# Performance work log

Measured on AMD Instinct MI355X. Metric: run time of the kernel, lower is better.

Reference implementation:

```python
import jax, jax.numpy as jnp
import numpy as np

KERNEL = 500
PAD_IDX = 256


def setup_inputs() -> dict:
    key = jax.random.key(0)
    ks = jax.random.split(key, 8)
    B, L = 8, 1_000_000
    x = jax.random.randint(ks[0], (B, L), 0, 257, dtype=jnp.int64)
    emb = jax.random.normal(ks[1], (257, 8), dtype=jnp.float32)
    emb = emb.at[PAD_IDX].set(0.0)  # padding_idx row is zero
    W1 = jax.random.normal(ks[2], (128, 8, KERNEL), dtype=jnp.float32) * 0.02
    b1 = jax.random.normal(ks[3], (128,), dtype=jnp.float32) * 0.02
    W2 = jax.random.normal(ks[4], (128, 8, KERNEL), dtype=jnp.float32) * 0.02
    b2 = jax.random.normal(ks[5], (128,), dtype=jnp.float32) * 0.02
    fcW = jax.random.normal(ks[6], (2, 128), dtype=jnp.float32) * 0.1
    fcb = jax.random.normal(ks[7], (2,), dtype=jnp.float32) * 0.1
    return {"x": x, "emb": emb, "W1": W1, "b1": b1, "W2": W2, "b2": b2, "fcW": fcW, "fcb": fcb}


def reference(x, emb, W1, b1, W2, b2, fcW, fcb):
    B, L = x.shape
    P = L // KERNEL  # non-overlapping patches (stride == kernel_size)
    # embedding with padding_idx semantics: output zero at pad positions
    e = emb[x] * (x != PAD_IDX)[..., None].astype(emb.dtype)  # [B, L, 8]
    patches = e.reshape(B, P, KERNEL, 8)                      # [B, P, K, C]
    # conv1d(k=stride=500) == patchified GEMM; weight layout [out, in, k]
    g1 = jnp.einsum('bpkc,ock->bpo', patches, W1) + b1        # [B, P, 128]
    g2 = jnp.einsum('bpkc,ock->bpo', patches, W2) + b2
    h = jax.nn.relu(g1 * jax.nn.sigmoid(g2))                  # GLU gate + relu
    m = jnp.max(h, axis=1)                                    # global max pool -> [B, 128]
    return m @ fcW.T + fcb                                    # [B, num_classes]
```

## Files before the change

### kernel.cpp

```cpp
#include <hip/hip_runtime.h>


typedef __attribute__((ext_vector_type(8))) short short8;
typedef __attribute__((ext_vector_type(4))) float f32x4;

__device__ __forceinline__ unsigned short f2b(float f) {
    union { float f; unsigned u; } un;
    un.f = f;
    unsigned u = un.u;
    return (unsigned short)((u + 0x7FFFu + ((u >> 16) & 1u)) >> 16);
}

#define KT_COUNT 125
#define WS_BBLK_BYTES (KT_COUNT * 256 * 32 * 2)
#define WS_MWS_OFF WS_BBLK_BYTES

__global__ __launch_bounds__(128) void prep_weights(
        const float* __restrict__ W1, const float* __restrict__ W2,
        unsigned short* __restrict__ Bblk, float* __restrict__ m_ws) {
    const int o  = blockIdx.x;
    const int kt = threadIdx.x;
    if (kt < KT_COUNT) {
        const float* W = (o < 128) ? W1 : W2;
        const int oo = o & 127;
        unsigned short v[32];
#pragma unroll
        for (int c = 0; c < 8; ++c) {
            float4 f = *(const float4*)&W[oo * 4000 + c * 500 + kt * 4];
            v[c]      = f2b(f.x);
            v[8 + c]  = f2b(f.y);
            v[16 + c] = f2b(f.z);
            v[24 + c] = f2b(f.w);
        }
        unsigned short* dst = Bblk + kt * 8192 + o * 32;
#pragma unroll
        for (int q = 0; q < 4; ++q) {
            uint4 p;
            p.x = (unsigned)v[q * 8 + 0] | ((unsigned)v[q * 8 + 1] << 16);
            p.y = (unsigned)v[q * 8 + 2] | ((unsigned)v[q * 8 + 3] << 16);
            p.z = (unsigned)v[q * 8 + 4] | ((unsigned)v[q * 8 + 5] << 16);
            p.w = (unsigned)v[q * 8 + 6] | ((unsigned)v[q * 8 + 7] << 16);
            *(uint4*)(dst + q * 8) = p;
        }
    }
    if (blockIdx.x == 0)
        for (int i = threadIdx.x; i < 8 * 128; i += 128) m_ws[i] = 0.f;
}

__global__ __launch_bounds__(512, 2) void malconv_main(
        const int* __restrict__ x, const float* __restrict__ emb,
        const float* __restrict__ b1, const float* __restrict__ b2,
        const unsigned short* __restrict__ Bblk, float* __restrict__ m_ws) {
    __shared__ __align__(16) unsigned short embb[257 * 8];
    __shared__ __align__(16) unsigned short Alds[2][64 * 40];
    __shared__ __align__(16) unsigned short xlds[64 * 500];

    const int t = threadIdx.x;
    const int m0 = blockIdx.x * 64;

    for (int e = t; e < 257 * 8; e += 512) embb[e] = f2b(emb[e]);
    {
        const int4* xg = (const int4*)(x + m0 * 500);
        for (int i = t; i < 8000; i += 512) {
            int4 v = xg[i];
            ushort4 s;
            s.x = (unsigned short)v.x; s.y = (unsigned short)v.y;
            s.z = (unsigned short)v.z; s.w = (unsigned short)v.w;
            *(ushort4*)&xlds[i * 4] = s;
        }
    }

    const int lane = t & 63, wave = t >> 6;
    const int quad = lane >> 4, l16 = lane & 15;
    const int mq   = wave >> 2, nq = wave & 3;

    const int ar = t >> 2, aj = t & 3;

    const unsigned short* bbase = Bblk + (nq * 32 + l16) * 32 + quad * 8;

    f32x4 acc[2][4];
#pragma unroll
    for (int mi = 0; mi < 2; ++mi)
#pragma unroll
        for (int ni = 0; ni < 4; ++ni) {
            f32x4 z = {0.f, 0.f, 0.f, 0.f};
            acc[mi][ni] = z;
        }

    __syncthreads();

    unsigned short xvn = 0;
    if (t < 256) {
        unsigned short xv = xlds[ar * 500 + aj];
        *(uint4*)&Alds[0][ar * 40 + aj * 8] = *(const uint4*)&embb[xv * 8];
        xvn = xlds[ar * 500 + 4 + aj];
    }
    short8 bcur[4], bnxt[4];
    bcur[0] = *(const short8*)(bbase);
    bcur[1] = *(const short8*)(bbase + 512);
    bcur[2] = *(const short8*)(bbase + 4096);
    bcur[3] = *(const short8*)(bbase + 4608);
    __syncthreads();

    for (int kt = 0; kt < KT_COUNT; ++kt) {
        const int cur = kt & 1;
        if (kt < KT_COUNT - 1) {
            const unsigned short* bb = bbase + (kt + 1) * 8192;
            bnxt[0] = *(const short8*)(bb);
            bnxt[1] = *(const short8*)(bb + 512);
            bnxt[2] = *(const short8*)(bb + 4096);
            bnxt[3] = *(const short8*)(bb + 4608);
        }
        short8 afrag[2];
#pragma unroll
        for (int mi = 0; mi < 2; ++mi)
            afrag[mi] = *(const short8*)
                &Alds[cur][(mq * 32 + mi * 16 + l16) * 40 + quad * 8];
        if (t < 256 && kt < KT_COUNT - 1) {
            *(uint4*)&Alds[cur ^ 1][ar * 40 + aj * 8] =
                *(const uint4*)&embb[xvn * 8];
            if (kt < KT_COUNT - 2) xvn = xlds[ar * 500 + (kt + 2) * 4 + aj];
        }
#pragma unroll
        for (int mi = 0; mi < 2; ++mi)
#pragma unroll
            for (int ni = 0; ni < 4; ++ni)
                acc[mi][ni] = __builtin_amdgcn_mfma_f32_16x16x32_bf16(
                    afrag[mi], bcur[ni], acc[mi][ni], 0, 0, 0);
#pragma unroll
        for (int ni = 0; ni < 4; ++ni) bcur[ni] = bnxt[ni];
        __syncthreads();
    }

    const int b0 = m0 / 2000;
    const int bsplit = (b0 + 1) * 2000;
    const bool crosses = (m0 + 63) >= bsplit;
#pragma unroll
    for (int ni = 0; ni < 2; ++ni) {
        int o = nq * 32 + ni * 16 + l16;
        float bb1 = b1[o], bb2 = b2[o];
        float mx0 = 0.f, mx1 = 0.f;
#pragma unroll
        for (int mi = 0; mi < 2; ++mi)
#pragma unroll
            for (int r = 0; r < 4; ++r) {
                int ml = mq * 32 + mi * 16 + quad * 4 + r;
                float g1 = acc[mi][ni][r] + bb1;
                float g2 = acc[mi][ni + 2][r] + bb2;
                float h = fmaxf(g1 / (1.f + __expf(-g2)), 0.f);
                if (m0 + ml >= bsplit) mx1 = fmaxf(mx1, h);
                else                   mx0 = fmaxf(mx0, h);
            }
        mx0 = fmaxf(mx0, __shfl_xor(mx0, 16));
        mx0 = fmaxf(mx0, __shfl_xor(mx0, 32));
        mx1 = fmaxf(mx1, __shfl_xor(mx1, 16));
        mx1 = fmaxf(mx1, __shfl_xor(mx1, 32));
        if (quad == 0) {
            atomicMax((int*)&m_ws[b0 * 128 + o], __float_as_int(mx0));
            if (crosses)
                atomicMax((int*)&m_ws[(b0 + 1) * 128 + o], __float_as_int(mx1));
        }
    }
}

__global__ void fc_kernel(const float* __restrict__ m_ws,
                          const float* __restrict__ fcW,
                          const float* __restrict__ fcb,
                          float* __restrict__ out) {
    int t = threadIdx.x;
    if (t < 16) {
        int b = t >> 1, j = t & 1;
        float s = 0.f;
        for (int o = 0; o < 128; ++o) s += m_ws[b * 128 + o] * fcW[j * 128 + o];
        out[t] = s + fcb[j];
    }
}

extern "C" void kernel_launch(void* const* d_in, const int* in_sizes, int n_in,
                              void* d_out, int out_size, void* d_ws, size_t ws_size,
                              hipStream_t stream) {
    const int*   x   = (const int*)d_in[0];
    const float* emb = (const float*)d_in[1];
    const float* W1  = (const float*)d_in[2];
    const float* b1  = (const float*)d_in[3];
    const float* W2  = (const float*)d_in[4];
    const float* b2  = (const float*)d_in[5];
    const float* fcW = (const float*)d_in[6];
    const float* fcb = (const float*)d_in[7];
    float* out = (float*)d_out;

    unsigned short* Bblk = (unsigned short*)d_ws;
    float* m_ws = (float*)((char*)d_ws + WS_MWS_OFF);

    prep_weights<<<256, 128, 0, stream>>>(W1, W2, Bblk, m_ws);
    malconv_main<<<250, 512, 0, stream>>>(x, emb, b1, b2, Bblk, m_ws);
    fc_kernel<<<1, 64, 0, stream>>>(m_ws, fcW, fcb, out);
}
```

Baseline: 151.4 us.

## Gather A fragments directly from LDS embedding table, drop per-iteration barrier

Each lane now looks up its MFMA A fragment straight from the bf16 embedding table in LDS, indexed by its own token, instead of staging the fragments through a shared double buffer. This removes the LDS write/read round trip and the __syncthreads in every K-step. The weight prefetch is deepened to two steps ahead, which costs more registers per thread. Each A fragment is now loaded by all 4 N-waves rather than once, so LDS gather traffic goes up.

```diff
diff --git a/kernel.cpp b/kernel.cpp
--- a/kernel.cpp
+++ b/kernel.cpp
@@ -52,7 +52,6 @@
         const float* __restrict__ b1, const float* __restrict__ b2,
         const unsigned short* __restrict__ Bblk, float* __restrict__ m_ws) {
     __shared__ __align__(16) unsigned short embb[257 * 8];
-    __shared__ __align__(16) unsigned short Alds[2][64 * 40];
     __shared__ __align__(16) unsigned short xlds[64 * 500];
 
     const int t = threadIdx.x;
@@ -74,7 +73,8 @@
     const int quad = lane >> 4, l16 = lane & 15;
     const int mq   = wave >> 2, nq = wave & 3;
 
-    const int ar = t >> 2, aj = t & 3;
+    const int xb0 = (mq * 32 + l16) * 500 + quad;
+    const int xb1 = xb0 + 16 * 500;
 
     const unsigned short* bbase = Bblk + (nq * 32 + l16) * 32 + quad * 8;
 
@@ -89,47 +89,46 @@
 
     __syncthreads();
 
-    unsigned short xvn = 0;
-    if (t < 256) {
-        unsigned short xv = xlds[ar * 500 + aj];
-        *(uint4*)&Alds[0][ar * 40 + aj * 8] = *(const uint4*)&embb[xv * 8];
-        xvn = xlds[ar * 500 + 4 + aj];
+    unsigned short xv0 = xlds[xb0], xv1 = xlds[xb1];
+    short8 acur0 = *(const short8*)&embb[xv0 * 8];
+    short8 acur1 = *(const short8*)&embb[xv1 * 8];
+    unsigned short xg0 = xlds[xb0 + 4],  xg1 = xlds[xb1 + 4];
+    unsigned short xn0 = xlds[xb0 + 8],  xn1 = xlds[xb1 + 8];
+    short8 bcur[4], bnxt[4], bfut[4];
+#pragma unroll
+    for (int ni = 0; ni < 4; ++ni) {
+        const int off = (ni & 1) * 512 + (ni >> 1) * 4096;
+        bcur[ni] = *(const short8*)(bbase + off);
+        bnxt[ni] = *(const short8*)(bbase + 8192 + off);
     }
-    short8 bcur[4], bnxt[4];
-    bcur[0] = *(const short8*)(bbase);
-    bcur[1] = *(const short8*)(bbase + 512);
-    bcur[2] = *(const short8*)(bbase + 4096);
-    bcur[3] = *(const short8*)(bbase + 4608);
-    __syncthreads();
 
     for (int kt = 0; kt < KT_COUNT; ++kt) {
-        const int cur = kt & 1;
-        if (kt < KT_COUNT - 1) {
-            const unsigned short* bb = bbase + (kt + 1) * 8192;
-            bnxt[0] = *(const short8*)(bb);
-            bnxt[1] = *(const short8*)(bb + 512);
-            bnxt[2] = *(const short8*)(bb + 4096);
-            bnxt[3] = *(const short8*)(bb + 4608);
+        {
+            int ktf = kt + 2; if (ktf > KT_COUNT - 1) ktf = KT_COUNT - 1;
+            const unsigned short* bb = bbase + ktf * 8192;
+            bfut[0] = *(const short8*)(bb);
+            bfut[1] = *(const short8*)(bb + 512);
+            bfut[2] = *(const short8*)(bb + 4096);
+            bfut[3] = *(const short8*)(bb + 4608);
         }
-        short8 afrag[2];
-#pragma unroll
-        for (int mi = 0; mi < 2; ++mi)
-            afrag[mi] = *(const short8*)
-                &Alds[cur][(mq * 32 + mi * 16 + l16) * 40 + quad * 8];
-        if (t < 256 && kt < KT_COUNT - 1) {
-            *(uint4*)&Alds[cur ^ 1][ar * 40 + aj * 8] =
-                *(const uint4*)&embb[xvn * 8];
-            if (kt < KT_COUNT - 2) xvn = xlds[ar * 500 + (kt + 2) * 4 + aj];
+        short8 anxt0 = *(const short8*)&embb[xg0 * 8];
+        short8 anxt1 = *(const short8*)&embb[xg1 * 8];
+        {
+            int ktx = kt + 3; if (ktx > KT_COUNT - 1) ktx = KT_COUNT - 1;
+            xg0 = xn0; xg1 = xn1;
+            xn0 = xlds[xb0 + ktx * 4];
+            xn1 = xlds[xb1 + ktx * 4];
         }
 #pragma unroll
-        for (int mi = 0; mi < 2; ++mi)
+        for (int ni = 0; ni < 4; ++ni) {
+            acc[0][ni] = __builtin_amdgcn_mfma_f32_16x16x32_bf16(
+                acur0, bcur[ni], acc[0][ni], 0, 0, 0);
+            acc[1][ni] = __builtin_amdgcn_mfma_f32_16x16x32_bf16(
+                acur1, bcur[ni], acc[1][ni], 0, 0, 0);
+        }
+        acur0 = anxt0; acur1 = anxt1;
 #pragma unroll
-            for (int ni = 0; ni < 4; ++ni)
-                acc[mi][ni] = __builtin_amdgcn_mfma_f32_16x16x32_bf16(
-                    afrag[mi], bcur[ni], acc[mi][ni], 0, 0, 0);
-#pragma unroll
-        for (int ni = 0; ni < 4; ++ni) bcur[ni] = bnxt[ni];
-        __syncthreads();
+        for (int ni = 0; ni < 4; ++ni) { bcur[ni] = bnxt[ni]; bnxt[ni] = bfut[ni]; }
     }
 
     const int b0 = m0 / 2000;
```

Measured after the change: 152.1 us. About the same (+0.5%).
